# Kernel optimization log

Hardware: AMD Instinct MI355X
Metric: run time of the kernel (lower is better)

## Reference

```python
import jax, jax.numpy as jnp
import numpy as np

EPS = 1e-08
K_N = 10
K_E = 10
F_DIM = 512
SCALE = F_DIM ** -0.5
N_NODES = 16384
N_EDGES = 2048


def layernorm(x, w, b):
    mu = x.mean(axis=-1, keepdims=True)
    var = x.var(axis=-1, keepdims=True)
    return (x - mu) * jax.lax.rsqrt(var + 1e-5) * w + b


def mask_attn(attn, k):
    # topk along last dim, scatter boolean mask, elementwise masking
    _, idx = jax.lax.top_k(attn, k)
    rows = jnp.arange(attn.shape[0])[:, None]
    mask = jnp.zeros(attn.shape, dtype=bool).at[rows, idx].set(True)
    return attn * mask


def setup_inputs() -> dict:
    key = jax.random.key(0)
    ks = jax.random.split(key, 12)
    d, h = F_DIM, 512  # hidden = max(f_dim, 128)
    w = 0.02  # weight init scale to keep softmax unsaturated
    return {
        'inputs': jax.random.normal(ks[0], (N_NODES, d), jnp.float32),
        'noise': jax.random.normal(ks[1], (N_EDGES, d), jnp.float32),
        'edges_mu': jax.random.normal(ks[2], (1, d), jnp.float32),
        'edges_logsigma': jnp.zeros((1, d), jnp.float32),
        'Wq': jax.random.normal(ks[3], (d, d), jnp.float32) * w,
        'bq': jnp.zeros((d,), jnp.float32),
        'Wk': jax.random.normal(ks[4], (d, d), jnp.float32) * w,
        'bk': jnp.zeros((d,), jnp.float32),
        'Wv': jax.random.normal(ks[5], (d, d), jnp.float32) * w,
        'bv': jnp.zeros((d,), jnp.float32),
        'W1': jax.random.normal(ks[6], (2 * d, h), jnp.float32) * w,
        'b1': jnp.zeros((h,), jnp.float32),
        'W2': jax.random.normal(ks[7], (h, d), jnp.float32) * w,
        'b2': jnp.zeros((d,), jnp.float32),
        'ln_in_w': jnp.ones((d,), jnp.float32),
        'ln_in_b': jnp.zeros((d,), jnp.float32),
        'ln_e_w': jnp.ones((d,), jnp.float32),
        'ln_e_b': jnp.zeros((d,), jnp.float32),
    }


def reference(inputs, noise, edges_mu, edges_logsigma, Wq, bq, Wk, bk, Wv, bv,
              W1, b1, W2, b2, ln_in_w, ln_in_b, ln_e_w, ln_e_b):
    relu = jax.nn.relu
    # slot init: mu + sigma * noise  -> [n_s, d]
    edges = edges_mu + jnp.exp(edges_logsigma) * noise
    x = layernorm(inputs, ln_in_w, ln_in_b)          # [n, d]
    k = relu(x @ Wk + bk)                            # [n, d]
    v = relu(x @ Wv + bv)                            # [n, d]
    # single iteration (iters=1)
    e = layernorm(edges, ln_e_w, ln_e_b)             # [n_s, d]
    q = relu(e @ Wq + bq)                            # [n_s, d]
    dots = (q @ k.T) * SCALE                         # [n_s, n]
    attn = jax.nn.softmax(dots, axis=1) + EPS
    attn = attn / attn.sum(axis=1, keepdims=True)
    attn = mask_attn(attn, K_N)
    updates = attn @ v                               # [n_s, d]
    e = jnp.concatenate([e, updates], axis=1)        # [n_s, 2d]
    e = relu(e @ W1 + b1) @ W2 + b2                  # mlp -> [n_s, d]
    q2 = x @ Wq + bq                                 # note: no activation here
    k2 = relu(e @ Wk + bk)                           # [n_s, d]
    dots2 = (q2 @ k2.T) * SCALE                      # [n, n_s]
    attn_v = jax.nn.softmax(dots2, axis=1)
    H = mask_attn(attn_v, K_E)
    return e, H, dots2
```

## Files before the change

kernel.cpp:

```cpp
#include <hip/hip_runtime.h>
#include <stdint.h>


#define NN 16384
#define NE 2048
#define TOPK 10

static const float SCALE_F = 0.04419417382415922f;
#define EPS_F 1e-8f

using bf16x8  = __attribute__((ext_vector_type(8))) __bf16;
using floatx4 = __attribute__((ext_vector_type(4))) float;

__device__ __forceinline__ unsigned f_as_u(float f) {
  union { float f; unsigned u; } v; v.f = f; return v.u;
}
__device__ __forceinline__ float u_as_f(unsigned u) {
  union { unsigned u; float f; } v; v.u = u; return v.f;
}
__device__ __forceinline__ unsigned short f2bf(float f) {
  unsigned u = f_as_u(f);
  unsigned r = u + 0x7fffu + ((u >> 16) & 1u);
  return (unsigned short)(r >> 16);
}
__device__ __forceinline__ float bf2f(unsigned short h) {
  return u_as_f(((unsigned)h) << 16);
}

__device__ __forceinline__ void glds16(const unsigned short* g, unsigned short* l) {
  __builtin_amdgcn_global_load_lds(
      (const __attribute__((address_space(1))) unsigned int*)g,
      (__attribute__((address_space(3))) unsigned int*)l, 16, 0, 0);
}

__device__ __forceinline__ unsigned fkey(float f) {
  unsigned u = f_as_u(f);
  return (u & 0x80000000u) ? ~u : (u | 0x80000000u);
}
__device__ __forceinline__ float funkey(unsigned k) {
  unsigned u = (k & 0x80000000u) ? (k ^ 0x80000000u) : ~k;
  return u_as_f(u);
}
__device__ __forceinline__ unsigned long long packkc(float v, int col) {
  return ((unsigned long long)fkey(v) << 32) | (unsigned)(~(unsigned)col);
}
__device__ __forceinline__ int unpack_col(unsigned long long w) {
  return (int)(~(unsigned)(w & 0xFFFFFFFFull));
}
__device__ __forceinline__ float unpack_val(unsigned long long w) {
  return funkey((unsigned)(w >> 32));
}
__device__ __forceinline__ unsigned long long shfl_xor_u64(unsigned long long x, int m) {
  unsigned lo = (unsigned)x, hi = (unsigned)(x >> 32);
  lo = __shfl_xor(lo, m, 64);
  hi = __shfl_xor(hi, m, 64);
  return ((unsigned long long)hi << 32) | lo;
}

__global__ void transpose_all_kernel(
    const float* __restrict__ Wk, const float* __restrict__ Wv,
    const float* __restrict__ Wq, unsigned short* __restrict__ WcatT,
    const float* __restrict__ W1, unsigned short* __restrict__ W1Th,
    unsigned short* __restrict__ W1Tl,
    const float* __restrict__ W2, unsigned short* __restrict__ W2Th,
    unsigned short* __restrict__ W2Tl) {
  __shared__ float tile[32][33];
  int z = blockIdx.z;
  if (z != 3 && blockIdx.y >= 16) return;
  const float* src;
  unsigned short* dhi;
  unsigned short* dlo;
  int K;
  if (z < 3) {
    src = z == 0 ? Wk : (z == 1 ? Wv : Wq);
    dhi = WcatT + (size_t)z * 512 * 512;
    dlo = nullptr; K = 512;
  } else if (z == 3) {
    src = W1; dhi = W1Th; dlo = W1Tl; K = 1024;
  } else {
    src = W2; dhi = W2Th; dlo = W2Tl; K = 512;
  }
  int n0 = blockIdx.x * 32, k0 = blockIdx.y * 32;
  int tx = threadIdx.x, ty = threadIdx.y;
  for (int r = ty; r < 32; r += 8)
    tile[r][tx] = src[(size_t)(k0 + r) * 512 + n0 + tx];
  __syncthreads();
  for (int r = ty; r < 32; r += 8) {
    float v = tile[tx][r];
    size_t o = (size_t)(n0 + r) * K + k0 + tx;
    unsigned short h = f2bf(v);
    dhi[o] = h;
    if (dlo) dlo[o] = f2bf(v - bf2f(h));
  }
}

__device__ __forceinline__ float block_sum_256(float v, float* sm4) {
#pragma unroll
  for (int off = 32; off; off >>= 1) v += __shfl_down(v, off, 64);
  __syncthreads();
  if ((threadIdx.x & 63) == 0) sm4[threadIdx.x >> 6] = v;
  __syncthreads();
  return (sm4[0] + sm4[1]) + (sm4[2] + sm4[3]);
}

__global__ __launch_bounds__(256) void ln_all_kernel(
    const float* __restrict__ in, const float* __restrict__ w,
    const float* __restrict__ b, unsigned short* __restrict__ out_hi,
    const float* __restrict__ noise, const float* __restrict__ mu_e,
    const float* __restrict__ ls_e, const float* __restrict__ we,
    const float* __restrict__ be, unsigned short* __restrict__ e1_hi,
    unsigned short* __restrict__ e1_lo) {
  __shared__ float sm4[4];
  int row = blockIdx.x, tid = threadIdx.x;
  if (row < NN) {
    const float* r = in + (size_t)row * 512;
    float x0 = r[tid], x1 = r[tid + 256];
    float mu = block_sum_256(x0 + x1, sm4) * (1.0f / 512.0f);
    float d0 = x0 - mu, d1 = x1 - mu;
    float var = block_sum_256(d0 * d0 + d1 * d1, sm4) * (1.0f / 512.0f);
    float rs = rsqrtf(var + 1e-5f);
    out_hi[(size_t)row * 512 + tid]       = f2bf(d0 * rs * w[tid] + b[tid]);
    out_hi[(size_t)row * 512 + tid + 256] = f2bf(d1 * rs * w[tid + 256] + b[tid + 256]);
  } else {
    row -= NN;
    const float* r = noise + (size_t)row * 512;
    float x0 = mu_e[tid] + expf(ls_e[tid]) * r[tid];
    float x1 = mu_e[tid + 256] + expf(ls_e[tid + 256]) * r[tid + 256];
    float mu = block_sum_256(x0 + x1, sm4) * (1.0f / 512.0f);
    float d0 = x0 - mu, d1 = x1 - mu;
    float var = block_sum_256(d0 * d0 + d1 * d1, sm4) * (1.0f / 512.0f);
    float rs = rsqrtf(var + 1e-5f);
    float y0 = d0 * rs * we[tid] + be[tid];
    float y1 = d1 * rs * we[tid + 256] + be[tid + 256];
    size_t o = (size_t)row * 1024;
    unsigned short h0 = f2bf(y0), h1 = f2bf(y1);
    e1_hi[o + tid] = h0;             e1_lo[o + tid] = f2bf(y0 - bf2f(h0));
    e1_hi[o + tid + 256] = h1;       e1_lo[o + tid + 256] = f2bf(y1 - bf2f(h1));
  }
}

#define GEMM128_CORE(A_, LDA_, B_, bm_, bn_, acc_, SMEM_)                      \
  unsigned short* As = (unsigned short*)(SMEM_);                               \
  unsigned short* Bs = (unsigned short*)(SMEM_) + 8192;                        \
  {                                                                            \
    int srow = tid >> 3;                                                       \
    int scol = ((tid ^ (tid >> 3)) & 7) << 3;                                  \
    const unsigned short* gA = (A_) + ((bm_) + srow) * (size_t)(LDA_) + scol;  \
    const unsigned short* gB = (B_) + ((bn_) + srow) * (size_t)512 + scol;     \
    unsigned short* dA = As + wave * 512;                                      \
    unsigned short* dB = Bs + wave * 512;                                      \
    int swz0 = (quad ^ (lrow & 7)) << 3;                                       \
    int swz1 = swz0 ^ 32;                                                      \
    int aoff0 = (wave * 32 + lrow) * 64;                                       \
    int aoff1 = aoff0 + 16 * 64;                                               \
    int boffl = lrow * 64;                                                     \
    for (int k0 = 0; k0 < 512; k0 += 64) {                                     \
      glds16(gA + k0, dA);                                                     \
      glds16(gA + 32 * (size_t)(LDA_) + k0, dA + 2048);                        \
      glds16(gA + 64 * (size_t)(LDA_) + k0, dA + 4096);                        \
      glds16(gA + 96 * (size_t)(LDA_) + k0, dA + 6144);                        \
      glds16(gB + k0, dB);                                                     \
      glds16(gB + 32 * 512 + k0, dB + 2048);                                   \
      glds16(gB + 64 * 512 + k0, dB + 4096);                                   \
      glds16(gB + 96 * 512 + k0, dB + 6144);                                   \
      __syncthreads();                                                         \
      bf16x8 af00 = *(const bf16x8*)&As[aoff0 + swz0];                         \
      bf16x8 af01 = *(const bf16x8*)&As[aoff0 + swz1];                         \
      bf16x8 af10 = *(const bf16x8*)&As[aoff1 + swz0];                         \
      bf16x8 af11 = *(const bf16x8*)&As[aoff1 + swz1];                         \
      _Pragma("unroll")                                                        \
      for (int t = 0; t < 8; ++t) {                                            \
        bf16x8 bf0 = *(const bf16x8*)&Bs[t * 1024 + boffl + swz0];             \
        bf16x8 bf1 = *(const bf16x8*)&Bs[t * 1024 + boffl + swz1];             \
        acc_[0][t] = __builtin_amdgcn_mfma_f32_16x16x32_bf16(af00, bf0, acc_[0][t], 0, 0, 0); \
        acc_[0][t] = __builtin_amdgcn_mfma_f32_16x16x32_bf16(af01, bf1, acc_[0][t], 0, 0, 0); \
        acc_[1][t] = __builtin_amdgcn_mfma_f32_16x16x32_bf16(af10, bf0, acc_[1][t], 0, 0, 0); \
        acc_[1][t] = __builtin_amdgcn_mfma_f32_16x16x32_bf16(af11, bf1, acc_[1][t], 0, 0, 0); \
      }                                                                        \
      __syncthreads();                                                         \
    }                                                                          \
  }

#define XCD_PANEL_MAP(mt_, nt_, owns_m_)                                       \
  int xcd = bid & 7, idx = bid >> 3;                                           \
  int per = ((owns_m_) ? (mt_) : (nt_)) >> 3;                                  \
  int pa = idx % per, pb = idx / per;                                          \
  bm = (size_t)((owns_m_) ? (xcd * per + pa) : pb) * 128;                      \
  bn = (size_t)((owns_m_) ? pb : (xcd * per + pa)) * 128;

__global__ __launch_bounds__(256) void gemm128_dots_kernel(
    const unsigned short* __restrict__ A, const unsigned short* __restrict__ B,
    float alpha, float* __restrict__ C, int ldc, int mt, int nt, int owns_m) {
  __shared__ __align__(16) char smem[33792];
  int tid = threadIdx.x, wave = tid >> 6, lane = tid & 63;
  int lrow = lane & 15, quad = lane >> 4;
  int bid = (int)blockIdx.x;
  size_t bm, bn;
  XCD_PANEL_MAP(mt, nt, owns_m)
  floatx4 zero4 = {0.f, 0.f, 0.f, 0.f};
  floatx4 acc[2][8];
#pragma unroll
  for (int i = 0; i < 2; ++i)
#pragma unroll
    for (int t = 0; t < 8; ++t) acc[i][t] = zero4;
  GEMM128_CORE(A, 512, B, bm, bn, acc, smem)
  __syncthreads();
  float* wb = (float*)smem + wave * (16 * 132);
#pragma unroll
  for (int i = 0; i < 2; ++i) {
#pragma unroll
    for (int t = 0; t < 8; ++t)
#pragma unroll
      for (int r = 0; r < 4; ++r)
        wb[(quad * 4 + r) * 132 + t * 16 + lrow] = acc[i][t][r] * alpha;
    __syncthreads();
    size_t rowbase = bm + wave * 32 + i * 16;
#pragma unroll
    for (int p = 0; p < 8; ++p) {
      int rr = p * 2 + (lane >> 5);
      float4 v = *(const float4*)&wb[rr * 132 + ((lane & 31) << 2)];
      *(float4*)&C[(rowbase + rr) * (size_t)ldc + bn + ((lane & 31) << 2)] = v;
    }
    __syncthreads();
  }
}

__global__ __launch_bounds__(256) void gemm128_kvq_kernel(
    const unsigned short* __restrict__ X, const unsigned short* __restrict__ E1,
    const unsigned short* __restrict__ B,
    const float* __restrict__ bk, const float* __restrict__ bv,
    const float* __restrict__ bq,
    unsigned short* __restrict__ khi, unsigned short* __restrict__ vhi,
    unsigned short* __restrict__ q2hi, unsigned short* __restrict__ qhi) {
  __shared__ __align__(16) char smem[32768];
  int tid = threadIdx.x, wave = tid >> 6, lane = tid & 63;
  int lrow = lane & 15, quad = lane >> 4;
  int bid = (int)blockIdx.x;
  size_t bm, bn;
  const unsigned short* Aptr;
  int lda;
  unsigned short* dst;
  const float* bias;
  bool relu;
  if (bid < 1536) {
    XCD_PANEL_MAP(128, 12, 1)
    Aptr = X; lda = 512;
    int mat = (int)(bn >> 9);
    bias = mat == 0 ? bk : (mat == 1 ? bv : bq);
    dst = mat == 0 ? khi : (mat == 1 ? vhi : q2hi);
    relu = mat < 2;
  } else {
    int qb = bid - 1536;
    bm = (size_t)(qb >> 2) * 128;
    bn = 1024 + (size_t)(qb & 3) * 128;
    Aptr = E1; lda = 1024;
    dst = qhi; bias = bq; relu = true;
  }
  int colbase = (int)(bn & 511);
  floatx4 zero4 = {0.f, 0.f, 0.f, 0.f};
  floatx4 acc[2][8];
#pragma unroll
  for (int i = 0; i < 2; ++i)
#pragma unroll
    for (int t = 0; t < 8; ++t) acc[i][t] = zero4;
  GEMM128_CORE(Aptr, lda, B, bm, bn, acc, smem)
  __syncthreads();
  unsigned short* wb = (unsigned short*)smem + wave * (16 * 136);
#pragma unroll
  for (int i = 0; i < 2; ++i) {
#pragma unroll
    for (int t = 0; t < 8; ++t) {
      float bvv = bias[colbase + t * 16 + lrow];
#pragma unroll
      for (int r = 0; r < 4; ++r) {
        float v = acc[i][t][r] + bvv;
        if (relu) v = fmaxf(v, 0.0f);
        wb[(quad * 4 + r) * 136 + t * 16 + lrow] = f2bf(v);
      }
    }
    __syncthreads();
    size_t rowbase = bm + wave * 32 + i * 16;
#pragma unroll
    for (int p = 0; p < 4; ++p) {
      int rr = p * 4 + (lane >> 4);
      uint4 v = *(const uint4*)&wb[rr * 136 + ((lane & 15) << 3)];
      *(uint4*)&dst[(rowbase + rr) * 512 + colbase + ((lane & 15) << 3)] = v;
    }
    __syncthreads();
  }
}

template <bool SPLIT, bool RELU, bool HAS_BIAS, bool WF32, bool WHI, bool WLO>
__global__ __launch_bounds__(256) void gemm64_kernel(
    const unsigned short* __restrict__ Ahi, const unsigned short* __restrict__ Alo, int lda,
    const unsigned short* __restrict__ Bhi, const unsigned short* __restrict__ Blo, int K,
    const float* __restrict__ bias, float alpha,
    float* __restrict__ Cf, int ldc,
    unsigned short* __restrict__ Chi, unsigned short* __restrict__ Clo, int ldcb) {
  __shared__ __align__(16) unsigned short AsH[64 * 32];
  __shared__ __align__(16) unsigned short BsH[64 * 32];
  __shared__ __align__(16) unsigned short AsL[64 * 32];
  __shared__ __align__(16) unsigned short BsL[64 * 32];
  int tid = threadIdx.x, wave = tid >> 6, lane = tid & 63;
  int lrow = lane & 15, quad = lane >> 4;
  size_t bm = (size_t)blockIdx.x * 64, bn = (size_t)blockIdx.y * 64;
  int row = tid >> 2, off = (tid & 3) << 3;
  size_t aoff = (bm + row) * (size_t)lda + off;
  size_t boff = (bn + row) * (size_t)K + off;

  floatx4 zero4 = {0.f, 0.f, 0.f, 0.f};
  floatx4 acc[4];
#pragma unroll
  for (int t = 0; t < 4; ++t) acc[t] = zero4;

  uint4 ah = *(const uint4*)(Ahi + aoff);
  uint4 bh = *(const uint4*)(Bhi + boff);
  uint4 al, bl;
  if (SPLIT) {
    al = *(const uint4*)(Alo + aoff);
    bl = *(const uint4*)(Blo + boff);
  }
  for (int k0 = 0; k0 < K; k0 += 32) {
    __syncthreads();
    *(uint4*)&AsH[tid * 8] = ah;
    *(uint4*)&BsH[tid * 8] = bh;
    if (SPLIT) {
      *(uint4*)&AsL[tid * 8] = al;
      *(uint4*)&BsL[tid * 8] = bl;
    }
    __syncthreads();
    if (k0 + 32 < K) {
      ah = *(const uint4*)(Ahi + aoff + k0 + 32);
      bh = *(const uint4*)(Bhi + boff + k0 + 32);
      if (SPLIT) {
        al = *(const uint4*)(Alo + aoff + k0 + 32);
        bl = *(const uint4*)(Blo + boff + k0 + 32);
      }
    }
    int ai = (wave * 16 + lrow) * 32 + quad * 8;
    bf16x8 aH = *(const bf16x8*)&AsH[ai];
    bf16x8 aL;
    if (SPLIT) aL = *(const bf16x8*)&AsL[ai];
#pragma unroll
    for (int t = 0; t < 4; ++t) {
      int bi = (t * 16 + lrow) * 32 + quad * 8;
      bf16x8 bH = *(const bf16x8*)&BsH[bi];
      acc[t] = __builtin_amdgcn_mfma_f32_16x16x32_bf16(aH, bH, acc[t], 0, 0, 0);
      if (SPLIT) {
        bf16x8 bL = *(const bf16x8*)&BsL[bi];
        acc[t] = __builtin_amdgcn_mfma_f32_16x16x32_bf16(aH, bL, acc[t], 0, 0, 0);
        acc[t] = __builtin_amdgcn_mfma_f32_16x16x32_bf16(aL, bH, acc[t], 0, 0, 0);
      }
    }
  }
  size_t row0 = bm + wave * 16 + quad * 4;
#pragma unroll
  for (int t = 0; t < 4; ++t) {
    int col = (int)bn + t * 16 + lrow;
    float bv = HAS_BIAS ? bias[col] : 0.0f;
#pragma unroll
    for (int r = 0; r < 4; ++r) {
      float v = acc[t][r] * alpha + bv;
      if (RELU) v = fmaxf(v, 0.0f);
      if (WF32) Cf[(row0 + r) * (size_t)ldc + col] = v;
      if (WHI) {
        unsigned short h = f2bf(v);
        Chi[(row0 + r) * (size_t)ldcb + col] = h;
        if (WLO) Clo[(row0 + r) * (size_t)ldcb + col] = f2bf(v - bf2f(h));
      }
    }
  }
}

#define INSERT4(lv, li, v, col)                                   \
  do {                                                            \
    if ((v) > lv[3]) {                                            \
      float cv_ = (v); int ci_ = (col);                           \
      _Pragma("unroll")                                           \
      for (int j_ = 0; j_ < 4; ++j_) {                            \
        bool sw_ = (cv_ > lv[j_]);                                \
        float tv_ = sw_ ? lv[j_] : cv_;                           \
        int ti_ = sw_ ? li[j_] : ci_;                              \
        lv[j_] = sw_ ? cv_ : lv[j_];                              \
        li[j_] = sw_ ? ci_ : li[j_];                              \
        cv_ = tv_; ci_ = ti_;                                     \
      }                                                           \
    }                                                             \
  } while (0)

__global__ __launch_bounds__(256) void attn1_kernel(
    const float* __restrict__ dots,
    const unsigned short* __restrict__ vhi,
    unsigned short* __restrict__ e1_hi, unsigned short* __restrict__ e1_lo) {
  __shared__ float sm_m[4], sm_s[4];
  __shared__ unsigned long long wbest[4];
  __shared__ unsigned long long wkey_s[TOPK];

  int tid = threadIdx.x, wave = tid >> 6, lane = tid & 63;
  int rowi = blockIdx.x;
  const float4* r4 = (const float4*)(dots + (size_t)rowi * NN);

  float lv[4]; int li[4];
#pragma unroll
  for (int j = 0; j < 4; ++j) { lv[j] = -INFINITY; li[j] = 0x7fffffff; }
  unsigned long long selmask = 0ull;
  int taken = 0;

  float m_loc = -INFINITY, s_loc = 0.0f;
  for (int i = 0; i < 16; ++i) {
    float4 q = r4[tid + (i << 8)];
#pragma unroll
    for (int c = 0; c < 4; ++c) {
      float v = (&q.x)[c];
      int col = ((tid + (i << 8)) << 2) + c;
      if (v > m_loc) {
        s_loc = s_loc * __expf(m_loc - v) + 1.0f;
        m_loc = v;
      } else {
        s_loc += __expf(v - m_loc);
      }
      INSERT4(lv, li, v, col);
    }
  }
#pragma unroll
  for (int sft = 32; sft; sft >>= 1) {
    float om = __shfl_xor(m_loc, sft, 64);
    float os = __shfl_xor(s_loc, sft, 64);
    float M = fmaxf(m_loc, om);
    s_loc = s_loc * __expf(m_loc - M) + os * __expf(om - M);
    m_loc = M;
  }
  if (lane == 0) { sm_m[wave] = m_loc; sm_s[wave] = s_loc; }
  __syncthreads();
  float M = fmaxf(fmaxf(sm_m[0], sm_m[1]), fmaxf(sm_m[2], sm_m[3]));
  float Z = sm_s[0] * __expf(sm_m[0] - M) + sm_s[1] * __expf(sm_m[1] - M) +
            sm_s[2] * __expf(sm_m[2] - M) + sm_s[3] * __expf(sm_m[3] - M);

  for (int rnd = 0; rnd < TOPK; ++rnd) {
    unsigned long long key;
    if (taken < 4) {
      key = packkc(lv[0], li[0]);
    } else {
      key = 0ull;
      for (int i = 0; i < 16; ++i) {
        float4 q = r4[tid + (i << 8)];
#pragma unroll
        for (int c = 0; c < 4; ++c) {
          int sl = i * 4 + c;
          if (!((selmask >> sl) & 1ull)) {
            int col = ((tid + (i << 8)) << 2) + c;
            unsigned long long kk = packkc((&q.x)[c], col);
            if (kk > key) key = kk;
          }
        }
      }
    }
#pragma unroll
    for (int sft = 32; sft; sft >>= 1) {
      unsigned long long ok = shfl_xor_u64(key, sft);
      if (ok > key) key = ok;
    }
    if (lane == 0) wbest[wave] = key;
    __syncthreads();
    unsigned long long w = wbest[0];
    if (wbest[1] > w) w = wbest[1];
    if (wbest[2] > w) w = wbest[2];
    if (wbest[3] > w) w = wbest[3];
    if (tid == 0) wkey_s[rnd] = w;
    int wcol = unpack_col(w);
    if (((wcol >> 2) & 255) == tid) {
      int sl = ((wcol >> 10) << 2) | (wcol & 3);
      selmask |= (1ull << sl);
      if (taken < 4) {
#pragma unroll
        for (int j = 0; j < 3; ++j) { lv[j] = lv[j + 1]; li[j] = li[j + 1]; }
      }
      ++taken;
    }
    __syncthreads();
  }

  const float inv_den = 1.0f / (1.0f + (float)NN * EPS_F);
  float invZ = 1.0f / Z;
  float u0 = 0.f, u1 = 0.f;
#pragma unroll
  for (int j = 0; j < TOPK; ++j) {
    unsigned long long w = wkey_s[j];
    int col = unpack_col(w);
    float val = unpack_val(w);
    float a = (__expf(val - M) * invZ + EPS_F) * inv_den;
    const unsigned short* vr = vhi + (size_t)col * 512;
    u0 += a * bf2f(vr[tid]);
    u1 += a * bf2f(vr[tid + 256]);
  }
  size_t o = (size_t)rowi * 1024 + 512;
  unsigned short h0 = f2bf(u0), h1 = f2bf(u1);
  e1_hi[o + tid] = h0;             e1_lo[o + tid] = f2bf(u0 - bf2f(h0));
  e1_hi[o + tid + 256] = h1;       e1_lo[o + tid + 256] = f2bf(u1 - bf2f(h1));
}

__global__ __launch_bounds__(256) void attn2_kernel(const float* __restrict__ dots2,
                                                    float* __restrict__ Hout) {
  int tid = threadIdx.x, wave = tid >> 6, lane = tid & 63;
  int rowi = blockIdx.x * 4 + wave;
  const float4* r4 = (const float4*)(dots2 + (size_t)rowi * NE);

  float d[32];
  float m = -INFINITY;
#pragma unroll
  for (int i = 0; i < 8; ++i) {
    float4 q = r4[lane + (i << 6)];
#pragma unroll
    for (int c = 0; c < 4; ++c) {
      d[i * 4 + c] = (&q.x)[c];
      m = fmaxf(m, d[i * 4 + c]);
    }
  }
#pragma unroll
  for (int sft = 32; sft; sft >>= 1) m = fmaxf(m, __shfl_xor(m, sft, 64));

  float s = 0.f;
#pragma unroll
  for (int j = 0; j < 32; ++j) { d[j] = __expf(d[j] - m); s += d[j]; }
#pragma unroll
  for (int sft = 32; sft; sft >>= 1) s += __shfl_xor(s, sft, 64);
  float invZ = 1.0f / s;

  float lv[4]; int li[4];
#pragma unroll
  for (int j = 0; j < 4; ++j) { lv[j] = -INFINITY; li[j] = 0x7fffffff; }
#pragma unroll
  for (int i = 0; i < 8; ++i) {
#pragma unroll
    for (int c = 0; c < 4; ++c) {
      int col = ((lane + (i << 6)) << 2) + c;
      INSERT4(lv, li, d[i * 4 + c], col);
    }
  }

  unsigned selmask = 0;
  int taken = 0;
  for (int rnd = 0; rnd < TOPK; ++rnd) {
    unsigned long long key;
    if (taken < 4) {
      key = packkc(lv[0], li[0]);
    } else {
      key = 0ull;
#pragma unroll
      for (int j = 0; j < 32; ++j) {
        if (!((selmask >> j) & 1u)) {
          int col = ((lane + ((j >> 2) << 6)) << 2) + (j & 3);
          unsigned long long kk = packkc(d[j], col);
          if (kk > key) key = kk;
        }
      }
    }
#pragma unroll
    for (int sft = 32; sft; sft >>= 1) {
      unsigned long long ok = shfl_xor_u64(key, sft);
      if (ok > key) key = ok;
    }
    int wcol = unpack_col(key);
    if (((wcol >> 2) & 63) == lane) {
      int sl = ((wcol >> 8) << 2) | (wcol & 3);
      selmask |= (1u << sl);
      if (taken < 4) {
#pragma unroll
        for (int j = 0; j < 3; ++j) { lv[j] = lv[j + 1]; li[j] = li[j + 1]; }
      }
      ++taken;
    }
  }

  float* hr = Hout + (size_t)rowi * NE;
#pragma unroll
  for (int i = 0; i < 8; ++i) {
    float4 o;
#pragma unroll
    for (int c = 0; c < 4; ++c) {
      int sl = i * 4 + c;
      (&o.x)[c] = ((selmask >> sl) & 1u) ? d[sl] * invZ : 0.0f;
    }
    ((float4*)hr)[lane + (i << 6)] = o;
  }
}

extern "C" void kernel_launch(void* const* d_in, const int* in_sizes, int n_in,
                              void* d_out, int out_size, void* d_ws, size_t ws_size,
                              hipStream_t stream) {
  (void)in_sizes; (void)n_in; (void)out_size; (void)ws_size;
  const float* inputs  = (const float*)d_in[0];
  const float* noise   = (const float*)d_in[1];
  const float* edges_mu = (const float*)d_in[2];
  const float* edges_ls = (const float*)d_in[3];
  const float* Wq = (const float*)d_in[4];
  const float* bq = (const float*)d_in[5];
  const float* Wk = (const float*)d_in[6];
  const float* bk = (const float*)d_in[7];
  const float* Wv = (const float*)d_in[8];
  const float* bv = (const float*)d_in[9];
  const float* W1 = (const float*)d_in[10];
  const float* b1 = (const float*)d_in[11];
  const float* W2 = (const float*)d_in[12];
  const float* b2 = (const float*)d_in[13];
  const float* ln_in_w = (const float*)d_in[14];
  const float* ln_in_b = (const float*)d_in[15];
  const float* ln_e_w = (const float*)d_in[16];
  const float* ln_e_b = (const float*)d_in[17];

  float* out_e  = (float*)d_out;
  float* out_H  = out_e + (size_t)NE * 512;
  float* out_d2 = out_H + (size_t)NN * NE;

  const size_t MB = 1024 * 1024;
  unsigned char* hb = (unsigned char*)out_H;
  unsigned short* x_hi  = (unsigned short*)(hb);
  unsigned short* k_hi  = (unsigned short*)(hb + 16 * MB);
  unsigned short* v_hi  = (unsigned short*)(hb + 32 * MB);
  unsigned short* q2_hi = (unsigned short*)(hb + 48 * MB);
  unsigned short* WcatT = (unsigned short*)(hb + 64 * MB);
  unsigned short* W1Th  = (unsigned short*)(hb + 66 * MB);
  unsigned short* W1Tl  = (unsigned short*)(hb + 67 * MB);
  unsigned short* W2Th  = (unsigned short*)(hb + 68 * MB);
  unsigned short* W2Tl  = (unsigned short*)(hb + 68 * MB + 512 * 1024);
  unsigned short* e1_hi = (unsigned short*)(hb + 70 * MB);
  unsigned short* e1_lo = (unsigned short*)(hb + 74 * MB);
  unsigned short* q_hi  = (unsigned short*)(hb + 78 * MB);
  unsigned short* h_hi  = (unsigned short*)(hb + 80 * MB);
  unsigned short* h_lo  = (unsigned short*)(hb + 82 * MB);
  unsigned short* e_hi  = (unsigned short*)(hb + 84 * MB);
  unsigned short* WkT   = WcatT;
  float* dots = out_d2;
  unsigned short* k2_hi = (unsigned short*)d_ws;

  dim3 tb(256);
  dim3 t32(32, 8);

  transpose_all_kernel<<<dim3(16, 32, 5), t32, 0, stream>>>(
      Wk, Wv, Wq, WcatT, W1, W1Th, W1Tl, W2, W2Th, W2Tl);
  ln_all_kernel<<<NN + NE, tb, 0, stream>>>(
      inputs, ln_in_w, ln_in_b, x_hi,
      noise, edges_mu, edges_ls, ln_e_w, ln_e_b, e1_hi, e1_lo);

  gemm128_kvq_kernel<<<dim3(1600), tb, 0, stream>>>(
      x_hi, e1_hi, WcatT, bk, bv, bq, k_hi, v_hi, q2_hi, q_hi);
  gemm128_dots_kernel<<<dim3(2048), tb, 0, stream>>>(
      q_hi, k_hi, SCALE_F, dots, NN, 16, 128, 0);
  attn1_kernel<<<NE, tb, 0, stream>>>(dots, v_hi, e1_hi, e1_lo);
  gemm64_kernel<true, true, true, false, true, true><<<dim3(32, 8), tb, 0, stream>>>(
      e1_hi, e1_lo, 1024, W1Th, W1Tl, 1024, b1, 1.f, nullptr, 0, h_hi, h_lo, 512);
  gemm64_kernel<true, false, true, true, true, false><<<dim3(32, 8), tb, 0, stream>>>(
      h_hi, h_lo, 512, W2Th, W2Tl, 512, b2, 1.f, out_e, 512, e_hi, nullptr, 512);
  gemm64_kernel<false, true, true, false, true, false><<<dim3(32, 8), tb, 0, stream>>>(
      e_hi, nullptr, 512, WkT, nullptr, 512, bk, 1.f, nullptr, 0, k2_hi, nullptr, 512);
  gemm128_dots_kernel<<<dim3(2048), tb, 0, stream>>>(
      q2_hi, k2_hi, SCALE_F, out_d2, NE, 128, 16, 1);
  attn2_kernel<<<NN / 4, tb, 0, stream>>>(out_d2, out_H);
}
```

Baseline: 547.2 us.

## Fuse per-tile softmax stats into dots GEMM and prune attn1 top-k scan

The first dots GEMM epilogue now computes a per-row, per-128-column-tile max and sum of exponentials and writes them to a stats buffer. attn1 rebuilds the softmax normaliser from these 128 partials instead of rereading the full 16384-wide row. It then scans only the tiles whose max is at least the 10th-largest tile max, which must contain the top-10. This removes most of attn1's full-row read and exp work, at the cost of extra shuffles and exps in the GEMM epilogue and a small stats buffer.

```diff
diff --git a/kernel.cpp b/kernel.cpp
--- a/kernel.cpp
+++ b/kernel.cpp
@@ -190,7 +190,8 @@
 
 __global__ __launch_bounds__(256) void gemm128_dots_kernel(
     const unsigned short* __restrict__ A, const unsigned short* __restrict__ B,
-    float alpha, float* __restrict__ C, int ldc, int mt, int nt, int owns_m) {
+    float alpha, float* __restrict__ C, int ldc, int mt, int nt, int owns_m,
+    float2* __restrict__ stats) {
   __shared__ __align__(16) char smem[33792];
   int tid = threadIdx.x, wave = tid >> 6, lane = tid & 63;
   int lrow = lane & 15, quad = lane >> 4;
@@ -222,6 +223,32 @@
       *(float4*)&C[(rowbase + rr) * (size_t)ldc + bn + ((lane & 31) << 2)] = v;
     }
     __syncthreads();
+  }
+  if (stats) {
+    int j = (int)(bn >> 7);
+#pragma unroll
+    for (int i = 0; i < 2; ++i) {
+#pragma unroll
+      for (int r = 0; r < 4; ++r) {
+        float mv = acc[i][0][r];
+#pragma unroll
+        for (int t = 1; t < 8; ++t) mv = fmaxf(mv, acc[i][t][r]);
+#pragma unroll
+        for (int sft = 1; sft < 16; sft <<= 1)
+          mv = fmaxf(mv, __shfl_xor(mv, sft, 64));
+        float m = mv * alpha;
+        float s = 0.f;
+#pragma unroll
+        for (int t = 0; t < 8; ++t)
+          s += __expf(acc[i][t][r] * alpha - m);
+#pragma unroll
+        for (int sft = 1; sft < 16; sft <<= 1) s += __shfl_xor(s, sft, 64);
+        if (lrow == 0) {
+          int row = (int)bm + wave * 32 + i * 16 + quad * 4 + r;
+          stats[(size_t)row * 128 + j] = make_float2(m, s);
+        }
+      }
+    }
   }
 }
 
@@ -390,68 +417,79 @@
 
 __global__ __launch_bounds__(256) void attn1_kernel(
     const float* __restrict__ dots,
+    const float2* __restrict__ stats,
     const unsigned short* __restrict__ vhi,
     unsigned short* __restrict__ e1_hi, unsigned short* __restrict__ e1_lo) {
-  __shared__ float sm_m[4], sm_s[4];
+  __shared__ float sm_m[128], sm_s[128];
+  __shared__ unsigned long long sm_key[128];
+  __shared__ int clist[128], jpos[128];
+  __shared__ int sh_c;
+  __shared__ float sh_red[4];
+  __shared__ float sh_M, sh_th;
   __shared__ unsigned long long wbest[4];
   __shared__ unsigned long long wkey_s[TOPK];
 
   int tid = threadIdx.x, wave = tid >> 6, lane = tid & 63;
   int rowi = blockIdx.x;
-  const float4* r4 = (const float4*)(dots + (size_t)rowi * NN);
+  const float* drow = dots + (size_t)rowi * NN;
+
+  if (tid < 128) {
+    float2 ms = stats[(size_t)rowi * 128 + tid];
+    sm_m[tid] = ms.x; sm_s[tid] = ms.y;
+    sm_key[tid] = packkc(ms.x, tid);
+  }
+  if (tid == 0) sh_c = 0;
+  __syncthreads();
+
+  if (tid < 128) {
+    unsigned long long mykey = sm_key[tid];
+    int cnt = 0;
+    for (int i = 0; i < 128; ++i) cnt += (sm_key[i] > mykey) ? 1 : 0;
+    if (cnt == 0) sh_M = sm_m[tid];
+    if (cnt == 9) sh_th = sm_m[tid];
+  }
+  __syncthreads();
+  float M = sh_M, th = sh_th;
+
+  float zp = (tid < 128) ? sm_s[tid] * __expf(sm_m[tid] - M) : 0.f;
+#pragma unroll
+  for (int off = 32; off; off >>= 1) zp += __shfl_down(zp, off, 64);
+  if (lane == 0) sh_red[wave] = zp;
+  if (tid < 128 && sm_m[tid] >= th) {
+    int p = atomicAdd(&sh_c, 1);
+    clist[p] = tid;
+    jpos[tid] = p;
+  }
+  __syncthreads();
+  float Z = (sh_red[0] + sh_red[1]) + (sh_red[2] + sh_red[3]);
+  int c = sh_c;
+  int nel = c << 7;
 
   float lv[4]; int li[4];
 #pragma unroll
   for (int j = 0; j < 4; ++j) { lv[j] = -INFINITY; li[j] = 0x7fffffff; }
+  for (int idx = tid; idx < nel; idx += 256) {
+    int jj = clist[idx >> 7];
+    int col = (jj << 7) + (idx & 127);
+    float v = drow[col];
+    INSERT4(lv, li, v, col);
+  }
+
   unsigned long long selmask = 0ull;
   int taken = 0;
-
-  float m_loc = -INFINITY, s_loc = 0.0f;
-  for (int i = 0; i < 16; ++i) {
-    float4 q = r4[tid + (i << 8)];
-#pragma unroll
-    for (int c = 0; c < 4; ++c) {
-      float v = (&q.x)[c];
-      int col = ((tid + (i << 8)) << 2) + c;
-      if (v > m_loc) {
-        s_loc = s_loc * __expf(m_loc - v) + 1.0f;
-        m_loc = v;
-      } else {
-        s_loc += __expf(v - m_loc);
-      }
-      INSERT4(lv, li, v, col);
-    }
-  }
-#pragma unroll
-  for (int sft = 32; sft; sft >>= 1) {
-    float om = __shfl_xor(m_loc, sft, 64);
-    float os = __shfl_xor(s_loc, sft, 64);
-    float M = fmaxf(m_loc, om);
-    s_loc = s_loc * __expf(m_loc - M) + os * __expf(om - M);
-    m_loc = M;
-  }
-  if (lane == 0) { sm_m[wave] = m_loc; sm_s[wave] = s_loc; }
-  __syncthreads();
-  float M = fmaxf(fmaxf(sm_m[0], sm_m[1]), fmaxf(sm_m[2], sm_m[3]));
-  float Z = sm_s[0] * __expf(sm_m[0] - M) + sm_s[1] * __expf(sm_m[1] - M) +
-            sm_s[2] * __expf(sm_m[2] - M) + sm_s[3] * __expf(sm_m[3] - M);
-
   for (int rnd = 0; rnd < TOPK; ++rnd) {
     unsigned long long key;
     if (taken < 4) {
       key = packkc(lv[0], li[0]);
     } else {
       key = 0ull;
-      for (int i = 0; i < 16; ++i) {
-        float4 q = r4[tid + (i << 8)];
-#pragma unroll
-        for (int c = 0; c < 4; ++c) {
-          int sl = i * 4 + c;
-          if (!((selmask >> sl) & 1ull)) {
-            int col = ((tid + (i << 8)) << 2) + c;
-            unsigned long long kk = packkc((&q.x)[c], col);
-            if (kk > key) key = kk;
-          }
+      int p = 0;
+      for (int idx = tid; idx < nel; idx += 256, ++p) {
+        if (!((selmask >> p) & 1ull)) {
+          int jj = clist[idx >> 7];
+          int col = (jj << 7) + (idx & 127);
+          unsigned long long kk = packkc(drow[col], col);
+          if (kk > key) key = kk;
         }
       }
     }
@@ -468,9 +506,9 @@
     if (wbest[3] > w) w = wbest[3];
     if (tid == 0) wkey_s[rnd] = w;
     int wcol = unpack_col(w);
-    if (((wcol >> 2) & 255) == tid) {
-      int sl = ((wcol >> 10) << 2) | (wcol & 3);
-      selmask |= (1ull << sl);
+    int widx = (jpos[wcol >> 7] << 7) + (wcol & 127);
+    if ((widx & 255) == tid) {
+      selmask |= (1ull << (widx >> 8));
       if (taken < 4) {
 #pragma unroll
         for (int j = 0; j < 3; ++j) { lv[j] = lv[j + 1]; li[j] = li[j + 1]; }
@@ -629,6 +667,7 @@
   unsigned short* h_hi  = (unsigned short*)(hb + 80 * MB);
   unsigned short* h_lo  = (unsigned short*)(hb + 82 * MB);
   unsigned short* e_hi  = (unsigned short*)(hb + 84 * MB);
+  float2* stats1        = (float2*)(hb + 86 * MB);
   unsigned short* WkT   = WcatT;
   float* dots = out_d2;
   unsigned short* k2_hi = (unsigned short*)d_ws;
@@ -645,8 +684,8 @@
   gemm128_kvq_kernel<<<dim3(1600), tb, 0, stream>>>(
       x_hi, e1_hi, WcatT, bk, bv, bq, k_hi, v_hi, q2_hi, q_hi);
   gemm128_dots_kernel<<<dim3(2048), tb, 0, stream>>>(
-      q_hi, k_hi, SCALE_F, dots, NN, 16, 128, 0);
-  attn1_kernel<<<NE, tb, 0, stream>>>(dots, v_hi, e1_hi, e1_lo);
+      q_hi, k_hi, SCALE_F, dots, NN, 16, 128, 0, stats1);
+  attn1_kernel<<<NE, tb, 0, stream>>>(dots, stats1, v_hi, e1_hi, e1_lo);
   gemm64_kernel<true, true, true, false, true, true><<<dim3(32, 8), tb, 0, stream>>>(
       e1_hi, e1_lo, 1024, W1Th, W1Tl, 1024, b1, 1.f, nullptr, 0, h_hi, h_lo, 512);
   gemm64_kernel<true, false, true, true, true, false><<<dim3(32, 8), tb, 0, stream>>>(
@@ -654,6 +693,6 @@
   gemm64_kernel<false, true, true, false, true, false><<<dim3(32, 8), tb, 0, stream>>>(
       e_hi, nullptr, 512, WkT, nullptr, 512, bk, 1.f, nullptr, 0, k2_hi, nullptr, 512);
   gemm128_dots_kernel<<<dim3(2048), tb, 0, stream>>>(
-      q2_hi, k2_hi, SCALE_F, out_d2, NE, 128, 16, 1);
+      q2_hi, k2_hi, SCALE_F, out_d2, NE, 128, 16, 1, nullptr);
   attn2_kernel<<<NN / 4, tb, 0, stream>>>(out_d2, out_H);
 }
```

Measured after the change: 551.6 us. Within noise of the previous version (+0.8%).
